# Optimization experiments

Measured on AMD Instinct MI355X. Metric: run time of the kernel, lower is better.

The kernel has to match this reference:

```python
import jax, jax.numpy as jnp
from jax import lax
import numpy as np

NUM_CENTERS = 2048
MAX_PER_GROUP = 32
NUM_FREQ = 10
BN_EPS = 1e-5


def setup_inputs() -> dict:
    key = jax.random.key(0)
    ks = jax.random.split(key, 8)
    N = 131072
    d = {}
    d['points'] = jax.random.normal(ks[0], (N, 2), dtype=jnp.float32) * 3.0
    d['W1'] = jax.random.normal(ks[1], (40, 64), dtype=jnp.float32) * (1.0 / np.sqrt(40))
    d['b1'] = jax.random.normal(ks[2], (64,), dtype=jnp.float32) * 0.01
    d['g1'] = jnp.ones((64,), jnp.float32)
    d['be1'] = jnp.zeros((64,), jnp.float32)
    d['W2'] = jax.random.normal(ks[3], (64, 128), dtype=jnp.float32) * (1.0 / np.sqrt(64))
    d['b2'] = jax.random.normal(ks[4], (128,), dtype=jnp.float32) * 0.01
    d['g2'] = jnp.ones((128,), jnp.float32)
    d['be2'] = jnp.zeros((128,), jnp.float32)
    d['W3'] = jax.random.normal(ks[5], (128, 16), dtype=jnp.float32) * (1.0 / np.sqrt(128))
    d['b3'] = jax.random.normal(ks[6], (16,), dtype=jnp.float32) * 0.01
    return d


def furthest_point_sampling(points, num_samples):
    # Sequential FPS; deterministic start at index 0 (torch version uses a random start).
    N = points.shape[0]
    dist0 = jnp.full((N,), jnp.inf, dtype=points.dtype)

    def step(carry, _):
        dist, cur = carry
        nd = jnp.linalg.norm(points - points[cur], axis=1)  # [N]
        dist = jnp.minimum(dist, nd)
        nxt = jnp.argmax(dist).astype(jnp.int32)
        dist = dist.at[nxt].set(0.0)
        return (dist, nxt), nxt

    (_, _), idxs = lax.scan(step, (dist0, jnp.int32(0)), None, length=num_samples - 1)
    return jnp.concatenate([jnp.zeros((1,), jnp.int32), idxs])


def group_points(points, centroids, K):
    # Assign each point to its nearest centroid, then pick up to K points per centroid
    # (deterministic: lowest indices first; torch picks a random subset when overfull).
    N = points.shape[0]
    M = centroids.shape[0]
    d2 = (jnp.sum(points ** 2, axis=1)[:, None]
          + jnp.sum(centroids ** 2, axis=1)[None, :]
          - 2.0 * points @ centroids.T)  # [N, M]
    assign = jnp.argmin(d2, axis=1)  # [N]
    mask = (assign[None, :] == jnp.arange(M, dtype=assign.dtype)[:, None])  # [M, N]
    # Earlier indices score higher so top_k returns assigned indices in ascending order.
    score = jnp.where(mask, (N - jnp.arange(N)).astype(jnp.int32)[None, :], jnp.int32(-1))
    _, sel = lax.top_k(score, K)  # [M, K]
    count = jnp.sum(mask, axis=1)  # [M]
    slot = jnp.arange(K)[None, :]
    valid = slot < count[:, None]
    last = jnp.take_along_axis(sel, jnp.clip(count - 1, 0, K - 1)[:, None], axis=1)  # [M,1]
    sel = jnp.where(valid, sel, last)  # pad with last assigned index
    grouped_pts = points[sel]  # [M, K, 2]
    empty = (count == 0)
    # Empty groups: slot 0 holds the centroid, rest zeros; indices all -1.
    slot0 = (slot == 0)[..., None]
    empty_pts = jnp.where(slot0, centroids[:, None, :], 0.0)
    grouped_pts = jnp.where(empty[:, None, None], empty_pts, grouped_pts)
    grouped_idx = jnp.where(empty[:, None], -1, sel)
    return grouped_idx, grouped_pts


def hf_encoding_2d(rel):
    # rel: [M, K, 2] -> [M, K, 4*NUM_FREQ], order: (freq, dim, [sin, cos])
    freqs = (2.0 ** jnp.arange(NUM_FREQ, dtype=rel.dtype)) * jnp.pi  # [F]
    ang = rel[:, :, None, :] * freqs[None, None, :, None]  # [M, K, F, 2]
    enc = jnp.stack([jnp.sin(ang), jnp.cos(ang)], axis=-1)  # [M, K, F, 2, 2]
    M, K = rel.shape[0], rel.shape[1]
    return enc.reshape(M, K, 4 * NUM_FREQ)


def batchnorm(x, g, b):
    mu = jnp.mean(x, axis=0)
    var = jnp.var(x, axis=0)
    return g * (x - mu) * lax.rsqrt(var + BN_EPS) + b


def reference(points, W1, b1, g1, be1, W2, b2, g2, be2, W3, b3):
    idx = furthest_point_sampling(points, NUM_CENTERS)
    centroids = points[idx]  # [M, 2]
    _, grouped_pts = group_points(points, centroids, MAX_PER_GROUP)
    rel = grouped_pts - centroids[:, None, :]  # [M, K, 2]
    enc = hf_encoding_2d(rel)  # [M, K, 40]
    M, K, D = enc.shape
    flat = enc.reshape(M * K, D)
    h = jax.nn.relu(batchnorm(flat @ W1 + b1, g1, be1))
    h = jax.nn.relu(batchnorm(h @ W2 + b2, g2, be2))
    out = (h @ W3 + b3).reshape(M, K, -1)
    features = jnp.max(out, axis=1)  # [M, output_dim]
    return features, centroids
```

## Files before the change

### kernel.cpp

```cpp
#include <hip/hip_runtime.h>
#include <hip/hip_bf16.h>
#include <math.h>

#define N_PTS   131072
#define M_CENT  2048
#define K_GRP   32
#define NSTEP   2047
#define NROWS   (M_CENT * K_GRP)
#define NCHUNK  512
#define BN_EPS  1e-5f

#define FPS_NB 32
#define FPS_NT 256
#define FPS_PPT (N_PTS / (FPS_NB * FPS_NT))
#define FPS_NW (FPS_NT / 64)
#define SLOT_STRIDE 16

__global__ __launch_bounds__(FPS_NT)
void fps_kernel(const float* __restrict__ pts, float* __restrict__ cents,
                float* __restrict__ outc, unsigned long long* __restrict__ slots) {
  const int b = blockIdx.x, t = threadIdx.x;
  const int lane = t & 63, wid = t >> 6;
  float px[FPS_PPT], py[FPS_PPT], dist[FPS_PPT];
  const int gbase = b * FPS_NT + t;
#pragma unroll
  for (int k = 0; k < FPS_PPT; k++) {
    int g = gbase + k * (FPS_NB * FPS_NT);
    px[k] = pts[2 * g]; py[k] = pts[2 * g + 1];
    dist[k] = __builtin_inff();
  }
  float cx = pts[0], cy = pts[1];
  if (b == 0 && t == 0) { cents[0] = cx; cents[1] = cy; outc[0] = cx; outc[1] = cy; }
  __shared__ unsigned long long lred[FPS_NW];
  __shared__ float s_cx, s_cy;

  for (int s = 0; s < NSTEP; s++) {
    const unsigned tag = (unsigned)(s + 1);
    float bestd = -1.0f; int bestk = 0;
#pragma unroll
    for (int k = 0; k < FPS_PPT; k++) {
      float dx = __fsub_rn(px[k], cx), dy = __fsub_rn(py[k], cy);
      float d2 = __fadd_rn(__fmul_rn(dx, dx), __fmul_rn(dy, dy));
      float nd = __fsqrt_rn(d2);
      float dm = fminf(dist[k], nd);
      dist[k] = dm;
      if (dm > bestd) { bestd = dm; bestk = k; }
    }
    const int bg = gbase + bestk * (FPS_NB * FPS_NT);
    unsigned long long key = ((unsigned long long)__float_as_uint(bestd) << 32)
                           | ((unsigned long long)tag << 17)
                           | (unsigned)(N_PTS - 1 - bg);
#pragma unroll
    for (int off = 32; off > 0; off >>= 1) {
      unsigned long long ok = __shfl_down(key, off);
      if (ok > key) key = ok;
    }
    if (lane == 0) lred[wid] = key;
    __syncthreads();
    if (wid == 0) {
      key = (lane < FPS_NW) ? lred[lane] : 0ull;
#pragma unroll
      for (int off = FPS_NW / 2; off > 0; off >>= 1) {
        unsigned long long ok = __shfl_down(key, off);
        if (ok > key) key = ok;
      }
      unsigned long long* sl = slots + (size_t)(s & 1) * FPS_NB * SLOT_STRIDE;
      if (lane == 0) {
        unsigned long long* ad = &sl[(size_t)b * SLOT_STRIDE];
        asm volatile("global_store_dwordx2 %0, %1, off sc0 sc1"
                     :: "v"(ad), "v"(key) : "memory");
      }
      unsigned long long gk = 0ull;
      if (lane < FPS_NB) {
        unsigned long long* ad = &sl[(size_t)lane * SLOT_STRIDE];
        unsigned long long v;
        for (;;) {
          asm volatile("global_load_dwordx2 %0, %1, off sc0 sc1\n\ts_waitcnt vmcnt(0)"
                       : "=v"(v) : "v"(ad) : "memory");
          if (((unsigned)v >> 17) == tag) break;
          __builtin_amdgcn_s_sleep(1);
        }
        gk = v;
      }
#pragma unroll
      for (int off = FPS_NB / 2; off > 0; off >>= 1) {
        unsigned long long ok = __shfl_down(gk, off);
        if (ok > gk) gk = ok;
      }
      if (lane == 0) {
        int idx = N_PTS - 1 - (int)(gk & 0x1FFFFull);
        float gx = pts[2 * idx], gy = pts[2 * idx + 1];
        s_cx = gx; s_cy = gy;
        if (b == 0) {
          cents[2 * (s + 1)] = gx; cents[2 * (s + 1) + 1] = gy;
          outc[2 * (s + 1)] = gx;  outc[2 * (s + 1) + 1] = gy;
        }
      }
    }
    __syncthreads();
    cx = s_cx; cy = s_cy;
  }
}

__global__ __launch_bounds__(256)
void assign_kernel(const float* __restrict__ pts, const float* __restrict__ cents,
                   int* __restrict__ assign) {
  __shared__ float scx[M_CENT], scy[M_CENT], sc2[M_CENT];
  const int t = threadIdx.x;
  for (int i = t; i < M_CENT; i += 256) {
    float x = cents[2 * i], y = cents[2 * i + 1];
    scx[i] = x; scy[i] = y;
    sc2[i] = __fadd_rn(__fmul_rn(x, x), __fmul_rn(y, y));
  }
  __syncthreads();
  const int n = blockIdx.x * 256 + t;
  float x = pts[2 * n], y = pts[2 * n + 1];
  float p2 = __fadd_rn(__fmul_rn(x, x), __fmul_rn(y, y));
  float best = __builtin_inff(); int bm = 0;
  for (int m = 0; m < M_CENT; m++) {
    float dot = __fadd_rn(__fmul_rn(x, scx[m]), __fmul_rn(y, scy[m]));
    float d2 = __fsub_rn(__fadd_rn(p2, sc2[m]), __fmul_rn(2.0f, dot));
    if (d2 < best) { best = d2; bm = m; }
  }
  assign[n] = bm;
}

__global__ __launch_bounds__(256)
void hist_kernel(const int* __restrict__ assign, unsigned* __restrict__ gcounts,
                 unsigned char* __restrict__ ranks) {
  __shared__ unsigned hist[M_CENT];
  __shared__ int sa[256];
  const int t = threadIdx.x, c = blockIdx.x;
  for (int i = t; i < M_CENT; i += 256) hist[i] = 0u;
  __syncthreads();
  const int n = c * 256 + t;
  const int m = assign[n];
  sa[t] = m;
  atomicAdd(&hist[m], 1u);
  __syncthreads();
  int r = 0;
  for (int j = 0; j < t; j++) r += (sa[j] == m);
  ranks[n] = (unsigned char)r;
  for (int i = t; i < M_CENT; i += 256) gcounts[(size_t)c * M_CENT + i] = hist[i];
}

__global__ __launch_bounds__(256)
void scan_kernel(unsigned* __restrict__ gcounts, unsigned* __restrict__ counts) {
  const int m = blockIdx.x * 256 + threadIdx.x;
  unsigned run = 0;
  for (int ch = 0; ch < NCHUNK; ch++) {
    unsigned v = gcounts[(size_t)ch * M_CENT + m];
    gcounts[(size_t)ch * M_CENT + m] = run;
    run += v;
  }
  counts[m] = run;
}

__global__ __launch_bounds__(256)
void scatter_kernel(const int* __restrict__ assign, const unsigned char* __restrict__ ranks,
                    const unsigned* __restrict__ gexcl, int* __restrict__ sel) {
  const int n = blockIdx.x * 256 + threadIdx.x;
  const int m = assign[n];
  unsigned pos = gexcl[(size_t)blockIdx.x * M_CENT + m] + (unsigned)ranks[n];
  if (pos < K_GRP) sel[m * K_GRP + pos] = n;
}

__global__ __launch_bounds__(256)
void encode_kernel(const float* __restrict__ pts, const float* __restrict__ cents,
                   const int* __restrict__ sel, const unsigned* __restrict__ counts,
                   float* __restrict__ enc) {
  const int tid = blockIdx.x * 256 + threadIdx.x;
  const int m = tid >> 5, k = tid & 31;
  const unsigned cnt = counts[m];
  const float cx = cents[2 * m], cy = cents[2 * m + 1];
  float rx, ry;
  if (cnt == 0u) {
    if (k == 0) { rx = 0.f; ry = 0.f; }
    else        { rx = 0.f - cx; ry = 0.f - cy; }
  } else {
    int kk = ((unsigned)k < cnt) ? k : (int)cnt - 1;
    int n = sel[m * K_GRP + kk];
    rx = __fsub_rn(pts[2 * n], cx);
    ry = __fsub_rn(pts[2 * n + 1], cy);
  }
  float row[40];
  float fr = 3.14159265358979323846f;
#pragma unroll
  for (int f = 0; f < 10; f++) {
    float ax = __fmul_rn(rx, fr), ay = __fmul_rn(ry, fr);
    float sx, cxs, sy, cys;
    sincosf(ax, &sx, &cxs);
    sincosf(ay, &sy, &cys);
    row[f * 4 + 0] = sx; row[f * 4 + 1] = cxs;
    row[f * 4 + 2] = sy; row[f * 4 + 3] = cys;
    fr = fr * 2.0f;
  }
  float4* dst = (float4*)(enc + (size_t)tid * 40);
#pragma unroll
  for (int i = 0; i < 10; i++)
    dst[i] = make_float4(row[4 * i], row[4 * i + 1], row[4 * i + 2], row[4 * i + 3]);
}

__global__ void zero_stats(float* __restrict__ s1, float* __restrict__ s2) {
  int t = threadIdx.x;
  if (t < 128) s1[t] = 0.f;
  s2[t] = 0.f;
}

__global__ __launch_bounds__(256)
void gemm1_stats(const float* __restrict__ enc, const float* __restrict__ W1,
                 const float* __restrict__ b1, float* __restrict__ stats1) {
  __shared__ float w1t[64 * 40];
  __shared__ float b1s[64];
  __shared__ float acc[128];
  const int t = threadIdx.x;
  for (int i = t; i < 2560; i += 256) { int c = i / 40, k = i % 40; w1t[i] = W1[k * 64 + c]; }
  if (t < 64) b1s[t] = b1[t];
  if (t < 128) acc[t] = 0.f;
  __syncthreads();
  const int row = blockIdx.x * 256 + t;
  const int lane = t & 63;
  float x[40];
  const float4* er = (const float4*)(enc + (size_t)row * 40);
#pragma unroll
  for (int i = 0; i < 10; i++) { float4 v = er[i]; x[4*i]=v.x; x[4*i+1]=v.y; x[4*i+2]=v.z; x[4*i+3]=v.w; }
  for (int c = 0; c < 64; c++) {
    float z = b1s[c];
    const float4* wc = (const float4*)(w1t + c * 40);
#pragma unroll
    for (int q = 0; q < 10; q++) {
      float4 w = wc[q];
      z += x[4*q]*w.x + x[4*q+1]*w.y + x[4*q+2]*w.z + x[4*q+3]*w.w;
    }
    float s = z, s2 = z * z;
#pragma unroll
    for (int off = 32; off > 0; off >>= 1) { s += __shfl_down(s, off); s2 += __shfl_down(s2, off); }
    if (lane == 0) { atomicAdd(&acc[c], s); atomicAdd(&acc[64 + c], s2); }
  }
  __syncthreads();
  if (t < 128) atomicAdd(&stats1[t], acc[t]);
}

__global__ void finalize_bn(const float* __restrict__ stats, const float* __restrict__ g,
                            const float* __restrict__ be, float* __restrict__ ab, int C) {
  int c = threadIdx.x;
  if (c < C) {
    const float invN = 1.0f / (float)NROWS;
    float mu = stats[c] * invN;
    float var = stats[C + c] * invN - mu * mu;
    float a = g[c] * rsqrtf(var + BN_EPS);
    ab[c] = a; ab[C + c] = be[c] - a * mu;
  }
}

__global__ __launch_bounds__(256)
void gemm2_stats(const float* __restrict__ enc, const float* __restrict__ W1,
                 const float* __restrict__ b1, const float* __restrict__ ab1,
                 const float* __restrict__ W2, const float* __restrict__ b2,
                 float* __restrict__ stats2) {
  __shared__ float w1t[64 * 40];
  __shared__ float w2t[128 * 64];
  __shared__ float b1s[64], b2s[128], ab1s[128];
  __shared__ float acc[256];
  const int t = threadIdx.x;
  for (int i = t; i < 2560; i += 256) { int c = i / 40, k = i % 40; w1t[i] = W1[k * 64 + c]; }
  for (int i = t; i < 8192; i += 256) { int c = i / 64, j = i % 64; w2t[i] = W2[j * 128 + c]; }
  if (t < 64) b1s[t] = b1[t];
  if (t < 128) { b2s[t] = b2[t]; ab1s[t] = ab1[t]; }
  if (t < 64) ab1s[64 + t] = ab1[64 + t];
  acc[t] = 0.f;
  __syncthreads();
  const int row = blockIdx.x * 256 + t;
  const int lane = t & 63;
  float x[40];
  const float4* er = (const float4*)(enc + (size_t)row * 40);
#pragma unroll
  for (int i = 0; i < 10; i++) { float4 v = er[i]; x[4*i]=v.x; x[4*i+1]=v.y; x[4*i+2]=v.z; x[4*i+3]=v.w; }
  float h[64];
  for (int c = 0; c < 64; c++) {
    float z = b1s[c];
    const float4* wc = (const float4*)(w1t + c * 40);
#pragma unroll
    for (int q = 0; q < 10; q++) {
      float4 w = wc[q];
      z += x[4*q]*w.x + x[4*q+1]*w.y + x[4*q+2]*w.z + x[4*q+3]*w.w;
    }
    h[c] = fmaxf(fmaf(ab1s[c], z, ab1s[64 + c]), 0.f);
  }
  for (int c = 0; c < 128; c++) {
    float z = b2s[c];
    const float4* wc = (const float4*)(w2t + c * 64);
#pragma unroll
    for (int q = 0; q < 16; q++) {
      float4 w = wc[q];
      z += h[4*q]*w.x + h[4*q+1]*w.y + h[4*q+2]*w.z + h[4*q+3]*w.w;
    }
    float s = z, s2 = z * z;
#pragma unroll
    for (int off = 32; off > 0; off >>= 1) { s += __shfl_down(s, off); s2 += __shfl_down(s2, off); }
    if (lane == 0) { atomicAdd(&acc[c], s); atomicAdd(&acc[128 + c], s2); }
  }
  __syncthreads();
  atomicAdd(&stats2[t], acc[t]);
}

__global__ __launch_bounds__(256)
void final_kernel(const float* __restrict__ enc, const float* __restrict__ W1,
                  const float* __restrict__ b1, const float* __restrict__ ab1,
                  const float* __restrict__ W2, const float* __restrict__ b2,
                  const float* __restrict__ ab2, const float* __restrict__ W3,
                  const float* __restrict__ b3, float* __restrict__ out_feat) {
  __shared__ float w1t[64 * 40];
  __shared__ float w2t[128 * 64];
  __shared__ float w3s[128 * 16];
  __shared__ float b1s[64], b2s[128], b3s[16], ab1s[128], ab2s[256];
  __shared__ float srow[256][16];
  const int t = threadIdx.x;
  for (int i = t; i < 2560; i += 256) { int c = i / 40, k = i % 40; w1t[i] = W1[k * 64 + c]; }
  for (int i = t; i < 8192; i += 256) { int c = i / 64, j = i % 64; w2t[i] = W2[j * 128 + c]; }
  for (int i = t; i < 2048; i += 256) w3s[i] = W3[i];
  if (t < 64) b1s[t] = b1[t];
  if (t < 128) { b2s[t] = b2[t]; ab1s[t] = ab1[t]; }
  if (t < 64) ab1s[64 + t] = ab1[64 + t];
  ab2s[t] = ab2[t];
  if (t < 16) b3s[t] = b3[t];
  __syncthreads();
  const int row = blockIdx.x * 256 + t;
  float x[40];
  const float4* er = (const float4*)(enc + (size_t)row * 40);
#pragma unroll
  for (int i = 0; i < 10; i++) { float4 v = er[i]; x[4*i]=v.x; x[4*i+1]=v.y; x[4*i+2]=v.z; x[4*i+3]=v.w; }
  float h[64];
  for (int c = 0; c < 64; c++) {
    float z = b1s[c];
    const float4* wc = (const float4*)(w1t + c * 40);
#pragma unroll
    for (int q = 0; q < 10; q++) {
      float4 w = wc[q];
      z += x[4*q]*w.x + x[4*q+1]*w.y + x[4*q+2]*w.z + x[4*q+3]*w.w;
    }
    h[c] = fmaxf(fmaf(ab1s[c], z, ab1s[64 + c]), 0.f);
  }
  float acc[16];
#pragma unroll
  for (int o = 0; o < 16; o++) acc[o] = b3s[o];
  for (int j = 0; j < 128; j++) {
    float z = b2s[j];
    const float4* wc = (const float4*)(w2t + j * 64);
#pragma unroll
    for (int q = 0; q < 16; q++) {
      float4 w = wc[q];
      z += h[4*q]*w.x + h[4*q+1]*w.y + h[4*q+2]*w.z + h[4*q+3]*w.w;
    }
    float h2 = fmaxf(fmaf(ab2s[j], z, ab2s[128 + j]), 0.f);
    const float4* w3r = (const float4*)(w3s + j * 16);
#pragma unroll
    for (int q = 0; q < 4; q++) {
      float4 w = w3r[q];
      acc[4*q] += h2 * w.x; acc[4*q+1] += h2 * w.y; acc[4*q+2] += h2 * w.z; acc[4*q+3] += h2 * w.w;
    }
  }
#pragma unroll
  for (int o = 0; o < 16; o++) srow[t][o] = acc[o];
  __syncthreads();
  if (t < 128) {
    const int g = t >> 4, c = t & 15;
    float mx = srow[g * 32][c];
#pragma unroll
    for (int r = 1; r < 32; r++) mx = fmaxf(mx, srow[g * 32 + r][c]);
    out_feat[(size_t)(blockIdx.x * 8 + g) * 16 + c] = mx;
  }
}

extern "C" void kernel_launch(void* const* d_in, const int* in_sizes, int n_in,
                              void* d_out, int out_size, void* d_ws, size_t ws_size,
                              hipStream_t stream) {
  const float* pts = (const float*)d_in[0];
  const float* W1 = (const float*)d_in[1];  const float* b1 = (const float*)d_in[2];
  const float* g1 = (const float*)d_in[3];  const float* be1 = (const float*)d_in[4];
  const float* W2 = (const float*)d_in[5];  const float* b2 = (const float*)d_in[6];
  const float* g2 = (const float*)d_in[7];  const float* be2 = (const float*)d_in[8];
  const float* W3 = (const float*)d_in[9];  const float* b3 = (const float*)d_in[10];
  float* out = (float*)d_out;

  char* w = (char*)d_ws;
  auto carve = [&](size_t bytes) -> char* {
    char* p = w;
    w += (bytes + 255) & ~(size_t)255;
    return p;
  };
  unsigned long long* slots = (unsigned long long*)carve((size_t)2 * FPS_NB * SLOT_STRIDE * 8);
  float*    cents  = (float*)carve((size_t)M_CENT * 2 * 4);
  int*      assign = (int*)carve((size_t)N_PTS * 4);
  unsigned char* ranks = (unsigned char*)carve((size_t)N_PTS);
  unsigned* gcounts = (unsigned*)carve((size_t)NCHUNK * M_CENT * 4);
  unsigned* counts  = (unsigned*)carve((size_t)M_CENT * 4);
  int*      sel     = (int*)carve((size_t)M_CENT * K_GRP * 4);
  float*    enc     = (float*)carve((size_t)NROWS * 40 * 4);
  float*    stats1  = (float*)carve(128 * 4);
  float*    stats2  = (float*)carve(256 * 4);
  float*    ab1     = (float*)carve(128 * 4);
  float*    ab2     = (float*)carve(256 * 4);

  float* out_feat = out;
  float* out_cent = out + (size_t)M_CENT * 16;

  hipLaunchKernelGGL(zero_stats, dim3(1), dim3(256), 0, stream, stats1, stats2);
  hipLaunchKernelGGL(fps_kernel, dim3(FPS_NB), dim3(FPS_NT), 0, stream,
                     pts, cents, out_cent, slots);
  hipLaunchKernelGGL(assign_kernel, dim3(N_PTS / 256), dim3(256), 0, stream,
                     pts, cents, assign);
  hipLaunchKernelGGL(hist_kernel, dim3(NCHUNK), dim3(256), 0, stream,
                     assign, gcounts, ranks);
  hipLaunchKernelGGL(scan_kernel, dim3(M_CENT / 256), dim3(256), 0, stream,
                     gcounts, counts);
  hipLaunchKernelGGL(scatter_kernel, dim3(NCHUNK), dim3(256), 0, stream,
                     assign, ranks, gcounts, sel);
  hipLaunchKernelGGL(encode_kernel, dim3(NROWS / 256), dim3(256), 0, stream,
                     pts, cents, sel, counts, enc);
  hipLaunchKernelGGL(gemm1_stats, dim3(NROWS / 256), dim3(256), 0, stream,
                     enc, W1, b1, stats1);
  hipLaunchKernelGGL(finalize_bn, dim3(1), dim3(64), 0, stream, stats1, g1, be1, ab1, 64);
  hipLaunchKernelGGL(gemm2_stats, dim3(NROWS / 256), dim3(256), 0, stream,
                     enc, W1, b1, ab1, W2, b2, stats2);
  hipLaunchKernelGGL(finalize_bn, dim3(1), dim3(128), 0, stream, stats2, g2, be2, ab2, 128);
  hipLaunchKernelGGL(final_kernel, dim3(NROWS / 256), dim3(256), 0, stream,
                     enc, W1, b1, ab1, W2, b2, ab2, W3, b3, out_feat);
}
```

Baseline: 5.259 ms.

## Restructure FPS to single-wave blocks, removing intra-block barriers and LDS reduction

The furthest-point-sampling kernel now runs 64 blocks of one wavefront each instead of 32 blocks of 256 threads. This removes the per-step LDS reduction and both __syncthreads barriers. Every lane now polls one slot in the cross-block exchange and does a butterfly xor reduction, so all lanes get the winning index without a shared-memory broadcast. The cost is twice as many blocks in the global spin-wait exchange, plus fixed s_sleep delays that could add latency to each of the 2047 sequential steps.

```diff
diff --git a/kernel.cpp b/kernel.cpp
--- a/kernel.cpp
+++ b/kernel.cpp
@@ -10,19 +10,18 @@
 #define NCHUNK  512
 #define BN_EPS  1e-5f
 
-#define FPS_NB 32
-#define FPS_NT 256
+#define FPS_NB 64
+#define FPS_NT 64
 #define FPS_PPT (N_PTS / (FPS_NB * FPS_NT))
-#define FPS_NW (FPS_NT / 64)
 #define SLOT_STRIDE 16
 
 __global__ __launch_bounds__(FPS_NT)
 void fps_kernel(const float* __restrict__ pts, float* __restrict__ cents,
                 float* __restrict__ outc, unsigned long long* __restrict__ slots) {
-  const int b = blockIdx.x, t = threadIdx.x;
-  const int lane = t & 63, wid = t >> 6;
+  const int b = blockIdx.x;
+  const int lane = threadIdx.x;
   float px[FPS_PPT], py[FPS_PPT], dist[FPS_PPT];
-  const int gbase = b * FPS_NT + t;
+  const int gbase = b * FPS_NT + lane;
 #pragma unroll
   for (int k = 0; k < FPS_PPT; k++) {
     int g = gbase + k * (FPS_NB * FPS_NT);
@@ -30,9 +29,7 @@
     dist[k] = __builtin_inff();
   }
   float cx = pts[0], cy = pts[1];
-  if (b == 0 && t == 0) { cents[0] = cx; cents[1] = cy; outc[0] = cx; outc[1] = cy; }
-  __shared__ unsigned long long lred[FPS_NW];
-  __shared__ float s_cx, s_cy;
+  if (b == 0 && lane == 0) { cents[0] = cx; cents[1] = cy; outc[0] = cx; outc[1] = cy; }
 
   for (int s = 0; s < NSTEP; s++) {
     const unsigned tag = (unsigned)(s + 1);
@@ -52,53 +49,37 @@
                            | (unsigned)(N_PTS - 1 - bg);
 #pragma unroll
     for (int off = 32; off > 0; off >>= 1) {
-      unsigned long long ok = __shfl_down(key, off);
+      unsigned long long ok = __shfl_xor(key, off);
       if (ok > key) key = ok;
     }
-    if (lane == 0) lred[wid] = key;
-    __syncthreads();
-    if (wid == 0) {
-      key = (lane < FPS_NW) ? lred[lane] : 0ull;
-#pragma unroll
-      for (int off = FPS_NW / 2; off > 0; off >>= 1) {
-        unsigned long long ok = __shfl_down(key, off);
-        if (ok > key) key = ok;
+    unsigned long long* sl = slots + (size_t)(s & 1) * FPS_NB * SLOT_STRIDE;
+    if (lane == 0) {
+      unsigned long long* ad = &sl[(size_t)b * SLOT_STRIDE];
+      asm volatile("global_store_dwordx2 %0, %1, off sc0 sc1"
+                   :: "v"(ad), "v"(key) : "memory");
+    }
+    __builtin_amdgcn_s_sleep(8);
+    unsigned long long gk;
+    {
+      unsigned long long* ad = &sl[(size_t)lane * SLOT_STRIDE];
+      for (;;) {
+        asm volatile("global_load_dwordx2 %0, %1, off sc0 sc1\n\ts_waitcnt vmcnt(0)"
+                     : "=v"(gk) : "v"(ad) : "memory");
+        if (((unsigned)gk >> 17) == tag) break;
+        __builtin_amdgcn_s_sleep(2);
       }
-      unsigned long long* sl = slots + (size_t)(s & 1) * FPS_NB * SLOT_STRIDE;
-      if (lane == 0) {
-        unsigned long long* ad = &sl[(size_t)b * SLOT_STRIDE];
-        asm volatile("global_store_dwordx2 %0, %1, off sc0 sc1"
-                     :: "v"(ad), "v"(key) : "memory");
-      }
-      unsigned long long gk = 0ull;
-      if (lane < FPS_NB) {
-        unsigned long long* ad = &sl[(size_t)lane * SLOT_STRIDE];
-        unsigned long long v;
-        for (;;) {
-          asm volatile("global_load_dwordx2 %0, %1, off sc0 sc1\n\ts_waitcnt vmcnt(0)"
-                       : "=v"(v) : "v"(ad) : "memory");
-          if (((unsigned)v >> 17) == tag) break;
-          __builtin_amdgcn_s_sleep(1);
-        }
-        gk = v;
-      }
-#pragma unroll
-      for (int off = FPS_NB / 2; off > 0; off >>= 1) {
-        unsigned long long ok = __shfl_down(gk, off);
-        if (ok > gk) gk = ok;
-      }
-      if (lane == 0) {
-        int idx = N_PTS - 1 - (int)(gk & 0x1FFFFull);
-        float gx = pts[2 * idx], gy = pts[2 * idx + 1];
-        s_cx = gx; s_cy = gy;
-        if (b == 0) {
-          cents[2 * (s + 1)] = gx; cents[2 * (s + 1) + 1] = gy;
-          outc[2 * (s + 1)] = gx;  outc[2 * (s + 1) + 1] = gy;
-        }
-      }
-    }
-    __syncthreads();
-    cx = s_cx; cy = s_cy;
+    }
+#pragma unroll
+    for (int off = 32; off > 0; off >>= 1) {
+      unsigned long long ok = __shfl_xor(gk, off);
+      if (ok > gk) gk = ok;
+    }
+    const int idx = N_PTS - 1 - (int)(gk & 0x1FFFFull);
+    cx = pts[2 * idx]; cy = pts[2 * idx + 1];
+    if (b == 0 && lane == 0) {
+      cents[2 * (s + 1)] = cx; cents[2 * (s + 1) + 1] = cy;
+      outc[2 * (s + 1)] = cx;  outc[2 * (s + 1) + 1] = cy;
+    }
   }
 }
 
```

After: 5.681 ms. +8.0%, slower.
